# Performance work log

Measured on AMD Instinct MI355X. Metric: run time of the kernel, lower is better.

## Reference

```python
import jax, jax.numpy as jnp
import numpy as np

B, T, F, E, H = 1024, 128, 32, 16, 20
EPS = 1e-3  # keras BatchNormalization default epsilon
D = T * F   # flatten dim; fc1 builds with units = T*F due to pre-build units mutation


def lstm_relu(x, Wk, Wr, b, return_seq):
    """Keras LSTM with activation='relu', recurrent_activation=sigmoid.
    Gate order i, f, c(g), o. x: [B,T,Fin]. Returns [B,T,H] or [B,H]."""
    Bn = x.shape[0]
    h0 = jnp.zeros((Bn, H), x.dtype)
    c0 = jnp.zeros((Bn, H), x.dtype)

    def step(carry, xt):
        h, c = carry
        z = xt @ Wk + h @ Wr + b                      # [B, 4H]
        i, f, g, o = jnp.split(z, 4, axis=-1)
        i = jax.nn.sigmoid(i)
        f = jax.nn.sigmoid(f)
        g = jax.nn.relu(g)
        o = jax.nn.sigmoid(o)
        c = f * c + i * g
        h = o * jax.nn.relu(c)
        return (h, c), h

    (hT, _), hs = jax.lax.scan(step, (h0, c0), jnp.swapaxes(x, 0, 1))
    return jnp.swapaxes(hs, 0, 1) if return_seq else hT


def setup_inputs():
    key = jax.random.key(0)
    ks = jax.random.split(key, 16)
    s = 0.1
    d = {}
    d["x"] = jax.random.normal(ks[0], (B, T, F), jnp.float32)
    # BatchNorm (inference: moving stats)
    d["bn_gamma"] = jnp.ones((F,), jnp.float32)
    d["bn_beta"] = jnp.zeros((F,), jnp.float32)
    d["bn_mean"] = jax.random.normal(ks[1], (F,), jnp.float32) * 0.1
    d["bn_var"] = jax.random.uniform(ks[2], (F,), jnp.float32, 0.5, 1.5)
    # Per-expert LSTM stacks (stacked over expert axis E)
    d["k1"] = jax.random.normal(ks[3], (E, F, 4 * H), jnp.float32) * s
    d["r1"] = jax.random.normal(ks[4], (E, H, 4 * H), jnp.float32) * s
    d["b1"] = jnp.zeros((E, 4 * H), jnp.float32)
    d["k2"] = jax.random.normal(ks[5], (E, H, 4 * H), jnp.float32) * s
    d["r2"] = jax.random.normal(ks[6], (E, H, 4 * H), jnp.float32) * s
    d["b2"] = jnp.zeros((E, 4 * H), jnp.float32)
    d["dw"] = jax.random.normal(ks[7], (E, H, 1), jnp.float32) * s
    d["db"] = jnp.zeros((E, 1), jnp.float32)
    # Gating path: flatten -> Dense(D, relu) -> Dense(E, softmax)
    d["fc1_w"] = jax.random.normal(ks[8], (D, D), jnp.float32) * 0.02
    d["fc1_b"] = jnp.zeros((D,), jnp.float32)
    d["gate_w"] = jax.random.normal(ks[9], (D, E), jnp.float32) * 0.02
    d["gate_b"] = jnp.zeros((E,), jnp.float32)
    return d


def reference(x, bn_gamma, bn_beta, bn_mean, bn_var,
              k1, r1, b1, k2, r2, b2, dw, db,
              fc1_w, fc1_b, gate_w, gate_b):
    # BatchNorm (inference) over last axis
    xn = (x - bn_mean) * jax.lax.rsqrt(bn_var + EPS) * bn_gamma + bn_beta

    def run_expert(k1e, r1e, b1e, k2e, r2e, b2e, dwe, dbe):
        h1 = lstm_relu(xn, k1e, r1e, b1e, return_seq=True)    # [B,T,H]
        h2 = lstm_relu(h1, k2e, r2e, b2e, return_seq=False)   # [B,H]
        return h2 @ dwe + dbe                                  # [B,1]

    expert_outputs = jax.vmap(run_expert)(k1, r1, b1, k2, r2, b2, dw, db)  # [E,B,1]

    flat = x.reshape(x.shape[0], -1)                    # [B, T*F] (raw inputs, not normed)
    g = jax.nn.relu(flat @ fc1_w + fc1_b)               # [B, D]
    w = jax.nn.softmax(g @ gate_w + gate_b, axis=-1)    # [B, E]

    # stack(axis=1) -> [B,E,1]; weights expand_dims(axis=2) -> [B,E,1]; sum over E
    out = jnp.sum(jnp.transpose(expert_outputs, (1, 0, 2)) * w[:, :, None], axis=1)  # [B,1]
    return out
```

## Files before the change

kernel.cpp:

```cpp
#include <hip/hip_runtime.h>
#include <math.h>

#define Bsz 1024
#define Tt  128
#define Ff  32
#define Ee  16
#define Hh  20
#define Dd  4096
#define EPSc 1e-3f
#define LOG2E 1.4426950408889634f

#define PWE 7520

typedef __attribute__((ext_vector_type(8))) short bf16x8;
typedef __attribute__((ext_vector_type(4))) float f32x4;
typedef __attribute__((ext_vector_type(4))) unsigned int u32x4;

#define MFMA16(a,b,c) __builtin_amdgcn_mfma_f32_16x16x32_bf16(a, b, c, 0, 0, 0)

__device__ __forceinline__ float sig2(float z) {
    return __builtin_amdgcn_rcpf(1.0f + __builtin_amdgcn_exp2f(-z));
}
__device__ __forceinline__ unsigned short bf16_rne(float f) {
    unsigned u = __float_as_uint(f);
    u += 0x7FFFu + ((u >> 16) & 1u);
    return (unsigned short)(u >> 16);
}
__device__ __forceinline__ float bf16_to_f(unsigned short h) {
    return __uint_as_float(((unsigned)h) << 16);
}
__device__ __forceinline__ void cvt2(float f0, float f1, unsigned& hp, unsigned& lp) {
    asm("v_cvt_pk_bf16_f32 %0, %1, %2" : "=v"(hp) : "v"(f0), "v"(f1));
    float h0 = __uint_as_float(hp << 16);
    float h1 = __uint_as_float(hp & 0xFFFF0000u);
    asm("v_cvt_pk_bf16_f32 %0, %1, %2" : "=v"(lp) : "v"(f0 - h0), "v"(f1 - h1));
}

__global__ void xpack_kernel(const float* __restrict__ x,
                             const float* __restrict__ gamma, const float* __restrict__ beta,
                             const float* __restrict__ mean,  const float* __restrict__ var,
                             unsigned short* __restrict__ xph, unsigned short* __restrict__ xpl)
{
    __shared__ float sc[Ff], sh[Ff];
    int tid = threadIdx.x;
    if (tid < Ff) {
        float s = gamma[tid] * rsqrtf(var[tid] + EPSc);
        sc[tid] = s;
        sh[tid] = beta[tid] - mean[tid] * s;
    }
    __syncthreads();
    int idx = blockIdx.x * 256 + tid;
    int c   = idx >> 13;
    int rem = idx & 8191;
    int t   = rem >> 6;
    int l   = rem & 63;
    int q   = l >> 4, s = l & 15;
    const float* xr = x + ((size_t)(c * 16 + s) * Tt + t) * Ff + q * 8;
    float4 v0 = *(const float4*)xr;
    float4 v1 = *(const float4*)(xr + 4);
    float xv[8] = {v0.x, v0.y, v0.z, v0.w, v1.x, v1.y, v1.z, v1.w};
    bf16x8 hv, lv;
#pragma unroll
    for (int j = 0; j < 8; ++j) {
        int f = q * 8 + j;
        float xn_ = xv[j] * sc[f] + sh[f];
        unsigned short hi = bf16_rne(xn_);
        hv[j] = (short)hi;
        lv[j] = (short)bf16_rne(xn_ - bf16_to_f(hi));
    }
    *(bf16x8*)(xph + (size_t)idx * 8) = hv;
    *(bf16x8*)(xpl + (size_t)idx * 8) = lv;
}

__global__ void repack2_kernel(const float* __restrict__ k1, const float* __restrict__ r1,
                               const float* __restrict__ b1, const float* __restrict__ k2,
                               const float* __restrict__ r2, const float* __restrict__ b2,
                               float* __restrict__ pw)
{
    int idx = blockIdx.x * blockDim.x + threadIdx.x;
    if (idx >= Ee * PWE) return;
    int e = idx / PWE;
    int o = idx % PWE;
    float v;
    int g;
    if (o < 7360) {
        int c = o % 80, u = c >> 2;
        g = c & 3;
        int co = g * 20 + u;
        if (o < 2560) {
            int kk = o / 80;
            v = k1[((size_t)e * Ff + kk) * 80 + co];
        } else if (o < 4160) {
            int kk = (o - 2560) / 80;
            v = r1[((size_t)e * Hh + kk) * 80 + co];
        } else if (o < 5760) {
            int kk = (o - 4160) / 80;
            v = k2[((size_t)e * Hh + kk) * 80 + co];
        } else {
            int kk = (o - 5760) / 80;
            v = r2[((size_t)e * Hh + kk) * 80 + co];
        }
    } else if (o < 7440) {
        int c = o - 7360, u = c >> 2;
        g = c & 3;
        v = b1[(size_t)e * 80 + g * 20 + u];
    } else {
        int c = o - 7440, u = c >> 2;
        g = c & 3;
        v = b2[(size_t)e * 80 + g * 20 + u];
    }
    if (g != 2) v *= LOG2E;
    pw[idx] = v;
}

__global__ __launch_bounds__(256, 2) void fused_kernel(
    const unsigned short* __restrict__ xph, const unsigned short* __restrict__ xpl,
    const float* __restrict__ pw, const float* __restrict__ dw, const float* __restrict__ db,
    float* __restrict__ eo,
    const float* __restrict__ x, const float* __restrict__ W,
    const float* __restrict__ bias, float* __restrict__ C)
{
    __shared__ __align__(16) char smem[32768];

    if (blockIdx.x < 256) {
        const int l = threadIdx.x & 63;
        const int q = l >> 4, s = l & 15;
        const int tile = (blockIdx.x << 2) + (threadIdx.x >> 6);
        const int e = tile >> 6;
        const int c = tile & 63;
        const int b0 = c * 16;

        const float* Wm = pw + (size_t)e * PWE;
        bf16x8 K1h[5], K1l[5], R1h[5], R1l[5], K2h[5], K2l[5], R2h[5], R2l[5];
#pragma unroll
        for (int n = 0; n < 5; ++n) {
#pragma unroll
            for (int j = 0; j < 8; ++j) {
                int k8 = q * 8 + j;
                int uk = 4 * j + q;
                int cc = n * 16 + s;
                float wv_;
                unsigned short hi; float hf;
                wv_ = Wm[k8 * 80 + cc];
                hi = bf16_rne(wv_); hf = bf16_to_f(hi);
                K1h[n][j] = (short)hi; K1l[n][j] = (short)bf16_rne(wv_ - hf);
                wv_ = (j < 5) ? Wm[2560 + uk * 80 + cc] : 0.f;
                hi = bf16_rne(wv_); hf = bf16_to_f(hi);
                R1h[n][j] = (short)hi; R1l[n][j] = (short)bf16_rne(wv_ - hf);
                wv_ = (j < 5) ? Wm[4160 + uk * 80 + cc] : 0.f;
                hi = bf16_rne(wv_); hf = bf16_to_f(hi);
                K2h[n][j] = (short)hi; K2l[n][j] = (short)bf16_rne(wv_ - hf);
                wv_ = (j < 5) ? Wm[5760 + uk * 80 + cc] : 0.f;
                hi = bf16_rne(wv_); hf = bf16_to_f(hi);
                R2h[n][j] = (short)hi; R2l[n][j] = (short)bf16_rne(wv_ - hf);
            }
        }
        f32x4 bf1[5], bf2[5];
        float dwr[5];
#pragma unroll
        for (int n = 0; n < 5; ++n) {
            bf1[n] = *(const f32x4*)&Wm[7360 + n * 16 + 4 * q];
            bf2[n] = *(const f32x4*)&Wm[7440 + n * 16 + 4 * q];
            dwr[n] = dw[e * Hh + 4 * n + q];
        }

        float c1[5] = {0, 0, 0, 0, 0}, c2[5] = {0, 0, 0, 0, 0};
        float h2reg[5] = {0, 0, 0, 0, 0};

        const bf16x8 z8 = {0, 0, 0, 0, 0, 0, 0, 0};
        bf16x8 H1a = z8, H1b = z8, H2a = z8, H2b = z8;

        const unsigned short* xbh = xph + (size_t)c * 65536 + l * 8;
        const unsigned short* xbl = xpl + (size_t)c * 65536 + l * 8;
        bf16x8 xch = *(const bf16x8*)xbh;
        bf16x8 xcl = *(const bf16x8*)xbl;

#pragma unroll 1
        for (int t = 0; t < Tt; ++t) {
            bf16x8 xnh = xch, xnl = xcl;
            if (t < Tt - 1) {
                xnh = *(const bf16x8*)(xbh + (t + 1) * 512);
                xnl = *(const bf16x8*)(xbl + (t + 1) * 512);
            }

            f32x4 a1[5];
#pragma unroll
            for (int n = 0; n < 5; ++n) {
                f32x4 acc = bf1[n];
                acc = MFMA16(K1h[n], xch, acc);
                acc = MFMA16(K1l[n], xch, acc);
                acc = MFMA16(K1h[n], xcl, acc);
                acc = MFMA16(R1h[n], H1a, acc);
                acc = MFMA16(R1l[n], H1a, acc);
                acc = MFMA16(R1h[n], H1b, acc);
                a1[n] = acc;
            }
            {
                float hv[5];
#pragma unroll
                for (int n = 0; n < 5; ++n) {
                    float iv = sig2(a1[n][0]);
                    float fv = sig2(a1[n][1]);
                    float gv = fmaxf(a1[n][2], 0.f);
                    float ov = sig2(a1[n][3]);
                    c1[n] = fv * c1[n] + iv * gv;
                    hv[n] = ov * fmaxf(c1[n], 0.f);
                }
                unsigned h0, h1, h2, l0, l1, l2;
                cvt2(hv[0], hv[1], h0, l0);
                cvt2(hv[2], hv[3], h1, l1);
                cvt2(hv[4], 0.f,   h2, l2);
                u32x4 uh = {h0, h1, h2, 0u}, ul = {l0, l1, l2, 0u};
                H1a = __builtin_bit_cast(bf16x8, uh);
                H1b = __builtin_bit_cast(bf16x8, ul);
            }

            f32x4 a2[5];
#pragma unroll
            for (int n = 0; n < 5; ++n) {
                f32x4 acc = bf2[n];
                acc = MFMA16(R2h[n], H2a, acc);
                acc = MFMA16(R2l[n], H2a, acc);
                acc = MFMA16(R2h[n], H2b, acc);
                acc = MFMA16(K2h[n], H1a, acc);
                acc = MFMA16(K2l[n], H1a, acc);
                acc = MFMA16(K2h[n], H1b, acc);
                a2[n] = acc;
            }
            {
                float hv[5];
#pragma unroll
                for (int n = 0; n < 5; ++n) {
                    float iv = sig2(a2[n][0]);
                    float fv = sig2(a2[n][1]);
                    float gv = fmaxf(a2[n][2], 0.f);
                    float ov = sig2(a2[n][3]);
                    c2[n] = fv * c2[n] + iv * gv;
                    float h = ov * fmaxf(c2[n], 0.f);
                    h2reg[n] = h;
                    hv[n] = h;
                }
                unsigned h0, h1, h2, l0, l1, l2;
                cvt2(hv[0], hv[1], h0, l0);
                cvt2(hv[2], hv[3], h1, l1);
                cvt2(hv[4], 0.f,   h2, l2);
                u32x4 uh = {h0, h1, h2, 0u}, ul = {l0, l1, l2, 0u};
                H2a = __builtin_bit_cast(bf16x8, uh);
                H2b = __builtin_bit_cast(bf16x8, ul);
            }

            xch = xnh; xcl = xnl;
        }

        float p = 0.f;
#pragma unroll
        for (int n = 0; n < 5; ++n) p += h2reg[n] * dwr[n];
        p += __shfl_xor(p, 16);
        p += __shfl_xor(p, 32);
        if (q == 0) eo[(size_t)e * Bsz + b0 + s] = db[e] + p;

    } else {
        const int tid = threadIdx.x;
        const int wv = tid >> 6, l = tid & 63, q = l >> 4, s = l & 15;
        const int id = blockIdx.x & 255;
        const int n0 = (id & 31) * 128, m0 = (id >> 5) * 128;
        const int wr = (wv & 1) * 64, wc = (wv >> 1) * 64;

        const int wn = tid & 127, wkq = tid >> 7;
        const int r7w = wn & 7;
        const int pw0 = ((2 * wkq)     ^ r7w) * 8;
        const int pw1 = ((2 * wkq + 1) ^ r7w) * 8;
        const int pw2 = ((4 + 2 * wkq) ^ r7w) * 8;
        const int pw3 = ((5 + 2 * wkq) ^ r7w) * 8;

        const float* WG = W + (size_t)(wkq * 16) * Dd + n0 + wn;
        const float* Arow = x + (size_t)(m0 + wr + s) * Dd + q * 8;

        unsigned short* lds = (unsigned short*)smem;

        f32x4 acc[4][4];
#pragma unroll
        for (int mt = 0; mt < 4; ++mt)
#pragma unroll
            for (int nt = 0; nt < 4; ++nt) acc[mt][nt] = (f32x4){0.f, 0.f, 0.f, 0.f};

        float wfp[16];
        float4 afc[8];

        {
            float w0[16];
#pragma unroll
            for (int i = 0; i < 16; ++i) w0[i] = WG[(size_t)i * Dd];
            uint4 h0, l0, h1, l1;
            cvt2(w0[0],  w0[1],  h0.x, l0.x); cvt2(w0[2],  w0[3],  h0.y, l0.y);
            cvt2(w0[4],  w0[5],  h0.z, l0.z); cvt2(w0[6],  w0[7],  h0.w, l0.w);
            cvt2(w0[8],  w0[9],  h1.x, l1.x); cvt2(w0[10], w0[11], h1.y, l1.y);
            cvt2(w0[12], w0[13], h1.z, l1.z); cvt2(w0[14], w0[15], h1.w, l1.w);
            unsigned short* rb = lds + wn * 64;
            *(uint4*)&rb[pw0] = h0;
            *(uint4*)&rb[pw1] = h1;
            *(uint4*)&rb[pw2] = l0;
            *(uint4*)&rb[pw3] = l1;
#pragma unroll
            for (int i = 0; i < 16; ++i) wfp[i] = WG[(size_t)(32 + i) * Dd];
#pragma unroll
            for (int mt = 0; mt < 4; ++mt) {
                afc[mt * 2]     = *(const float4*)(Arow + (size_t)mt * 16 * Dd);
                afc[mt * 2 + 1] = *(const float4*)(Arow + (size_t)mt * 16 * Dd + 4);
            }
            __syncthreads();
        }

#pragma unroll 1
        for (int it = 0; it < 128; ++it) {
            const int k0 = it * 32;
            unsigned short* cb = lds + (it & 1) * 8192;
            unsigned short* sb = lds + ((it & 1) ^ 1) * 8192;

            if (it < 127) {
                uint4 h0, l0, h1, l1;
                cvt2(wfp[0],  wfp[1],  h0.x, l0.x); cvt2(wfp[2],  wfp[3],  h0.y, l0.y);
                cvt2(wfp[4],  wfp[5],  h0.z, l0.z); cvt2(wfp[6],  wfp[7],  h0.w, l0.w);
                cvt2(wfp[8],  wfp[9],  h1.x, l1.x); cvt2(wfp[10], wfp[11], h1.y, l1.y);
                cvt2(wfp[12], wfp[13], h1.z, l1.z); cvt2(wfp[14], wfp[15], h1.w, l1.w);
                unsigned short* rb = sb + wn * 64;
                *(uint4*)&rb[pw0] = h0;
                *(uint4*)&rb[pw1] = h1;
                *(uint4*)&rb[pw2] = l0;
                *(uint4*)&rb[pw3] = l1;
            }

            {
                const int kW = (it + 2 < 128) ? k0 + 64 : k0;
#pragma unroll
                for (int i = 0; i < 16; ++i) wfp[i] = WG[(size_t)(kW + i) * Dd];
            }

            bf16x8 Wfh[4], Wfl[4];
            {
                const int r7r = s & 7;
                const int ph = (q ^ r7r) * 8;
                const int pl = ((4 + q) ^ r7r) * 8;
#pragma unroll
                for (int nt = 0; nt < 4; ++nt) {
                    const unsigned short* rb = cb + (wc + nt * 16 + s) * 64;
                    Wfh[nt] = *(bf16x8*)&rb[ph];
                    Wfl[nt] = *(bf16x8*)&rb[pl];
                }
            }

            bf16x8 Afh[4], Afl[4];
#pragma unroll
            for (int mt = 0; mt < 4; ++mt) {
                uint4 uh, ul;
                cvt2(afc[mt * 2].x,     afc[mt * 2].y,     uh.x, ul.x);
                cvt2(afc[mt * 2].z,     afc[mt * 2].w,     uh.y, ul.y);
                cvt2(afc[mt * 2 + 1].x, afc[mt * 2 + 1].y, uh.z, ul.z);
                cvt2(afc[mt * 2 + 1].z, afc[mt * 2 + 1].w, uh.w, ul.w);
                Afh[mt] = __builtin_bit_cast(bf16x8, uh);
                Afl[mt] = __builtin_bit_cast(bf16x8, ul);
            }
            {
                const int kA = (it + 1 < 128) ? k0 + 32 : k0;
#pragma unroll
                for (int mt = 0; mt < 4; ++mt) {
                    afc[mt * 2]     = *(const float4*)(Arow + (size_t)mt * 16 * Dd + kA);
                    afc[mt * 2 + 1] = *(const float4*)(Arow + (size_t)mt * 16 * Dd + kA + 4);
                }
            }

#pragma unroll
            for (int mt = 0; mt < 4; ++mt)
#pragma unroll
                for (int nt = 0; nt < 4; ++nt) {
                    f32x4 a = acc[mt][nt];
                    a = MFMA16(Afl[mt], Wfh[nt], a);
                    a = MFMA16(Afh[mt], Wfl[nt], a);
                    a = MFMA16(Afh[mt], Wfh[nt], a);
                    acc[mt][nt] = a;
                }

            __syncthreads();
        }

#pragma unroll
        for (int nt = 0; nt < 4; ++nt) {
            float bv = bias[n0 + wc + nt * 16 + s];
#pragma unroll
            for (int mt = 0; mt < 4; ++mt)
#pragma unroll
                for (int r = 0; r < 4; ++r) {
                    int m = m0 + wr + mt * 16 + q * 4 + r;
                    C[(size_t)m * Dd + n0 + wc + nt * 16 + s] = fmaxf(acc[mt][nt][r] + bv, 0.f);
                }
        }
    }
}

__global__ __launch_bounds__(256) void gate_kernel(const float* __restrict__ g,
                                                   const float* __restrict__ gw,
                                                   const float* __restrict__ gb,
                                                   const float* __restrict__ eo,
                                                   float* __restrict__ out)
{
    int b0 = blockIdx.x * 4;
    int tid = threadIdx.x;
    int lane = tid & 63;
    int wv = tid >> 6;

    float acc[4][16];
#pragma unroll
    for (int bb = 0; bb < 4; ++bb)
#pragma unroll
        for (int j = 0; j < 16; ++j) acc[bb][j] = 0.f;

    const float* g0 = g + (size_t)b0 * Dd;
#pragma unroll
    for (int it = 0; it < Dd / 256; ++it) {
        int d = tid + it * 256;
        const float4* wr_ = (const float4*)(gw + (size_t)d * 16);
        float4 w0 = wr_[0], w1 = wr_[1], w2 = wr_[2], w3 = wr_[3];
        float gv[4];
#pragma unroll
        for (int bb = 0; bb < 4; ++bb) gv[bb] = g0[(size_t)bb * Dd + d];
#pragma unroll
        for (int bb = 0; bb < 4; ++bb) {
            float v = gv[bb];
            acc[bb][0]  += v * w0.x;  acc[bb][1]  += v * w0.y;
            acc[bb][2]  += v * w0.z;  acc[bb][3]  += v * w0.w;
            acc[bb][4]  += v * w1.x;  acc[bb][5]  += v * w1.y;
            acc[bb][6]  += v * w1.z;  acc[bb][7]  += v * w1.w;
            acc[bb][8]  += v * w2.x;  acc[bb][9]  += v * w2.y;
            acc[bb][10] += v * w2.z;  acc[bb][11] += v * w2.w;
            acc[bb][12] += v * w3.x;  acc[bb][13] += v * w3.y;
            acc[bb][14] += v * w3.z;  acc[bb][15] += v * w3.w;
        }
    }

    __shared__ float red[4][4][16];
    __shared__ float logits[4][16];
#pragma unroll
    for (int bb = 0; bb < 4; ++bb)
#pragma unroll
        for (int j = 0; j < 16; ++j) {
            float v = acc[bb][j];
#pragma unroll
            for (int m = 32; m >= 1; m >>= 1) v += __shfl_xor(v, m);
            if (lane == 0) red[wv][bb][j] = v;
        }
    __syncthreads();
    if (tid < 64) {
        int bb = tid >> 4, j = tid & 15;
        logits[bb][j] = gb[j] + red[0][bb][j] + red[1][bb][j] + red[2][bb][j] + red[3][bb][j];
    }
    __syncthreads();
    if (tid < 4) {
        int b = b0 + tid;
        float m = logits[tid][0];
#pragma unroll
        for (int j = 1; j < 16; ++j) m = fmaxf(m, logits[tid][j]);
        float ex[16], ssum = 0.f;
#pragma unroll
        for (int j = 0; j < 16; ++j) { ex[j] = __expf(logits[tid][j] - m); ssum += ex[j]; }
        float inv = 1.f / ssum;
        float o = 0.f;
#pragma unroll
        for (int j = 0; j < 16; ++j) o += ex[j] * inv * eo[(size_t)j * Bsz + b];
        out[b] = o;
    }
}

extern "C" void kernel_launch(void* const* d_in, const int* in_sizes, int n_in,
                              void* d_out, int out_size, void* d_ws, size_t ws_size,
                              hipStream_t stream)
{
    const float* x     = (const float*)d_in[0];
    const float* gamma = (const float*)d_in[1];
    const float* beta  = (const float*)d_in[2];
    const float* mean  = (const float*)d_in[3];
    const float* var   = (const float*)d_in[4];
    const float* k1    = (const float*)d_in[5];
    const float* r1    = (const float*)d_in[6];
    const float* b1    = (const float*)d_in[7];
    const float* k2    = (const float*)d_in[8];
    const float* r2    = (const float*)d_in[9];
    const float* b2    = (const float*)d_in[10];
    const float* dw    = (const float*)d_in[11];
    const float* db    = (const float*)d_in[12];
    const float* fc1w  = (const float*)d_in[13];
    const float* fc1b  = (const float*)d_in[14];
    const float* gw    = (const float*)d_in[15];
    const float* gb    = (const float*)d_in[16];
    float* out = (float*)d_out;

    float* g = (float*)d_ws;
    unsigned short* xph = (unsigned short*)(g + (size_t)Bsz * Dd);
    unsigned short* xpl = xph + (size_t)Bsz * Dd / 2 * 2;
    float* pw  = (float*)(xpl + (size_t)4194304);
    float* eo  = pw + (size_t)Ee * PWE;

    xpack_kernel<<<2048, 256, 0, stream>>>(x, gamma, beta, mean, var, xph, xpl);
    repack2_kernel<<<(Ee * PWE + 255) / 256, 256, 0, stream>>>(k1, r1, b1, k2, r2, b2, pw);
    fused_kernel<<<512, 256, 0, stream>>>(xph, xpl, pw, dw, db, eo, x, fc1w, fc1b, g);
    gate_kernel<<<Bsz / 4, 256, 0, stream>>>(g, gw, gb, eo, out);
}
```

Baseline: 450.0 us.

## Stage GEMM A tiles through LDS with deeper prefetch and merge prep kernels

The fc1 GEMM path now converts and stages the A operand (raw x) into LDS alongside W, rather than each wave converting its own A fragments from registers. Global loads run two k-steps ahead using two register sets, with the loop unrolled by two over double-buffered LDS. The LDS allocation doubles to 64KB and register pressure rises, which can reduce occupancy for the LSTM blocks that share this kernel. The xpack and weight repack kernels are also merged into a single launch to save one kernel launch.

```diff
diff --git a/kernel.cpp b/kernel.cpp
--- a/kernel.cpp
+++ b/kernel.cpp
@@ -36,81 +36,81 @@
     asm("v_cvt_pk_bf16_f32 %0, %1, %2" : "=v"(lp) : "v"(f0 - h0), "v"(f1 - h1));
 }
 
-__global__ void xpack_kernel(const float* __restrict__ x,
-                             const float* __restrict__ gamma, const float* __restrict__ beta,
-                             const float* __restrict__ mean,  const float* __restrict__ var,
-                             unsigned short* __restrict__ xph, unsigned short* __restrict__ xpl)
+__global__ void prep_kernel(const float* __restrict__ x,
+                            const float* __restrict__ gamma, const float* __restrict__ beta,
+                            const float* __restrict__ mean,  const float* __restrict__ var,
+                            unsigned short* __restrict__ xph, unsigned short* __restrict__ xpl,
+                            const float* __restrict__ k1, const float* __restrict__ r1,
+                            const float* __restrict__ b1, const float* __restrict__ k2,
+                            const float* __restrict__ r2, const float* __restrict__ b2,
+                            float* __restrict__ pw)
 {
-    __shared__ float sc[Ff], sh[Ff];
     int tid = threadIdx.x;
-    if (tid < Ff) {
-        float s = gamma[tid] * rsqrtf(var[tid] + EPSc);
-        sc[tid] = s;
-        sh[tid] = beta[tid] - mean[tid] * s;
+    if (blockIdx.x < 2048) {
+        __shared__ float sc[Ff], sh[Ff];
+        if (tid < Ff) {
+            float s = gamma[tid] * rsqrtf(var[tid] + EPSc);
+            sc[tid] = s;
+            sh[tid] = beta[tid] - mean[tid] * s;
+        }
+        __syncthreads();
+        int idx = blockIdx.x * 256 + tid;
+        int c   = idx >> 13;
+        int rem = idx & 8191;
+        int t   = rem >> 6;
+        int l   = rem & 63;
+        int q   = l >> 4, s = l & 15;
+        const float* xr = x + ((size_t)(c * 16 + s) * Tt + t) * Ff + q * 8;
+        float4 v0 = *(const float4*)xr;
+        float4 v1 = *(const float4*)(xr + 4);
+        float xv[8] = {v0.x, v0.y, v0.z, v0.w, v1.x, v1.y, v1.z, v1.w};
+        bf16x8 hv, lv;
+#pragma unroll
+        for (int j = 0; j < 8; ++j) {
+            int f = q * 8 + j;
+            float xn_ = xv[j] * sc[f] + sh[f];
+            unsigned short hi = bf16_rne(xn_);
+            hv[j] = (short)hi;
+            lv[j] = (short)bf16_rne(xn_ - bf16_to_f(hi));
+        }
+        *(bf16x8*)(xph + (size_t)idx * 8) = hv;
+        *(bf16x8*)(xpl + (size_t)idx * 8) = lv;
+    } else {
+        int idx = (blockIdx.x - 2048) * 256 + tid;
+        if (idx >= Ee * PWE) return;
+        int e = idx / PWE;
+        int o = idx % PWE;
+        float v;
+        int g;
+        if (o < 7360) {
+            int c = o % 80, u = c >> 2;
+            g = c & 3;
+            int co = g * 20 + u;
+            if (o < 2560) {
+                int kk = o / 80;
+                v = k1[((size_t)e * Ff + kk) * 80 + co];
+            } else if (o < 4160) {
+                int kk = (o - 2560) / 80;
+                v = r1[((size_t)e * Hh + kk) * 80 + co];
+            } else if (o < 5760) {
+                int kk = (o - 4160) / 80;
+                v = k2[((size_t)e * Hh + kk) * 80 + co];
+            } else {
+                int kk = (o - 5760) / 80;
+                v = r2[((size_t)e * Hh + kk) * 80 + co];
+            }
+        } else if (o < 7440) {
+            int c = o - 7360, u = c >> 2;
+            g = c & 3;
+            v = b1[(size_t)e * 80 + g * 20 + u];
+        } else {
+            int c = o - 7440, u = c >> 2;
+            g = c & 3;
+            v = b2[(size_t)e * 80 + g * 20 + u];
+        }
+        if (g != 2) v *= LOG2E;
+        pw[idx] = v;
     }
-    __syncthreads();
-    int idx = blockIdx.x * 256 + tid;
-    int c   = idx >> 13;
-    int rem = idx & 8191;
-    int t   = rem >> 6;
-    int l   = rem & 63;
-    int q   = l >> 4, s = l & 15;
-    const float* xr = x + ((size_t)(c * 16 + s) * Tt + t) * Ff + q * 8;
-    float4 v0 = *(const float4*)xr;
-    float4 v1 = *(const float4*)(xr + 4);
-    float xv[8] = {v0.x, v0.y, v0.z, v0.w, v1.x, v1.y, v1.z, v1.w};
-    bf16x8 hv, lv;
-#pragma unroll
-    for (int j = 0; j < 8; ++j) {
-        int f = q * 8 + j;
-        float xn_ = xv[j] * sc[f] + sh[f];
-        unsigned short hi = bf16_rne(xn_);
-        hv[j] = (short)hi;
-        lv[j] = (short)bf16_rne(xn_ - bf16_to_f(hi));
-    }
-    *(bf16x8*)(xph + (size_t)idx * 8) = hv;
-    *(bf16x8*)(xpl + (size_t)idx * 8) = lv;
-}
-
-__global__ void repack2_kernel(const float* __restrict__ k1, const float* __restrict__ r1,
-                               const float* __restrict__ b1, const float* __restrict__ k2,
-                               const float* __restrict__ r2, const float* __restrict__ b2,
-                               float* __restrict__ pw)
-{
-    int idx = blockIdx.x * blockDim.x + threadIdx.x;
-    if (idx >= Ee * PWE) return;
-    int e = idx / PWE;
-    int o = idx % PWE;
-    float v;
-    int g;
-    if (o < 7360) {
-        int c = o % 80, u = c >> 2;
-        g = c & 3;
-        int co = g * 20 + u;
-        if (o < 2560) {
-            int kk = o / 80;
-            v = k1[((size_t)e * Ff + kk) * 80 + co];
-        } else if (o < 4160) {
-            int kk = (o - 2560) / 80;
-            v = r1[((size_t)e * Hh + kk) * 80 + co];
-        } else if (o < 5760) {
-            int kk = (o - 4160) / 80;
-            v = k2[((size_t)e * Hh + kk) * 80 + co];
-        } else {
-            int kk = (o - 5760) / 80;
-            v = r2[((size_t)e * Hh + kk) * 80 + co];
-        }
-    } else if (o < 7440) {
-        int c = o - 7360, u = c >> 2;
-        g = c & 3;
-        v = b1[(size_t)e * 80 + g * 20 + u];
-    } else {
-        int c = o - 7440, u = c >> 2;
-        g = c & 3;
-        v = b2[(size_t)e * 80 + g * 20 + u];
-    }
-    if (g != 2) v *= LOG2E;
-    pw[idx] = v;
 }
 
 __global__ __launch_bounds__(256, 2) void fused_kernel(
@@ -120,7 +120,7 @@
     const float* __restrict__ x, const float* __restrict__ W,
     const float* __restrict__ bias, float* __restrict__ C)
 {
-    __shared__ __align__(16) char smem[32768];
+    __shared__ __align__(16) char smem[65536];
 
     if (blockIdx.x < 256) {
         const int l = threadIdx.x & 63;
@@ -272,11 +272,21 @@
         const int pw1 = ((2 * wkq + 1) ^ r7w) * 8;
         const int pw2 = ((4 + 2 * wkq) ^ r7w) * 8;
         const int pw3 = ((5 + 2 * wkq) ^ r7w) * 8;
-
         const float* WG = W + (size_t)(wkq * 16) * Dd + n0 + wn;
-        const float* Arow = x + (size_t)(m0 + wr + s) * Dd + q * 8;
+
+        const int ar = tid >> 3, ac = tid & 7;
+        const int akc = ac >> 1, ahalf = ac & 1;
+        const int pa_h = ((akc       ^ (ar & 7)) << 3) + ahalf * 4;
+        const int pa_l = (((4 + akc) ^ (ar & 7)) << 3) + ahalf * 4;
+        const float* AG = x + (size_t)(m0 + ar) * Dd + 4 * ac;
+
+        const int r7r = s & 7;
+        const int pfh = (q ^ r7r) * 8;
+        const int pfl = ((4 + q) ^ r7r) * 8;
 
         unsigned short* lds = (unsigned short*)smem;
+        unsigned short* c0 = lds;
+        unsigned short* c1 = lds + 16384;
 
         f32x4 acc[4][4];
 #pragma unroll
@@ -284,104 +294,108 @@
 #pragma unroll
             for (int nt = 0; nt < 4; ++nt) acc[mt][nt] = (f32x4){0.f, 0.f, 0.f, 0.f};
 
-        float wfp[16];
-        float4 afc[8];
+        float wA[16], wB[16];
+        float4 aA[4], aB[4];
+
+#define LOADW(dst, kk)                                                     \
+        {                                                                  \
+            const int kw_ = (kk);                                          \
+            _Pragma("unroll")                                              \
+            for (int i_ = 0; i_ < 16; ++i_)                                \
+                dst[i_] = WG[(size_t)(kw_ + i_) * Dd];                     \
+        }
+#define LOADA(dst, kk)                                                     \
+        {                                                                  \
+            const int ka_ = (kk);                                          \
+            _Pragma("unroll")                                              \
+            for (int p_ = 0; p_ < 4; ++p_)                                 \
+                dst[p_] = *(const float4*)(AG + (size_t)(32 * p_) * Dd + ka_); \
+        }
+#define STAGEW(dst, src)                                                   \
+        {                                                                  \
+            uint4 h0, l0, h1, l1;                                          \
+            cvt2(src[0],  src[1],  h0.x, l0.x); cvt2(src[2],  src[3],  h0.y, l0.y); \
+            cvt2(src[4],  src[5],  h0.z, l0.z); cvt2(src[6],  src[7],  h0.w, l0.w); \
+            cvt2(src[8],  src[9],  h1.x, l1.x); cvt2(src[10], src[11], h1.y, l1.y); \
+            cvt2(src[12], src[13], h1.z, l1.z); cvt2(src[14], src[15], h1.w, l1.w); \
+            unsigned short* rb_ = (dst) + wn * 64;                         \
+            *(uint4*)&rb_[pw0] = h0;                                       \
+            *(uint4*)&rb_[pw1] = h1;                                       \
+            *(uint4*)&rb_[pw2] = l0;                                       \
+            *(uint4*)&rb_[pw3] = l1;                                       \
+        }
+#define STAGEA(dst, src)                                                   \
+        {                                                                  \
+            _Pragma("unroll")                                              \
+            for (int p_ = 0; p_ < 4; ++p_) {                               \
+                unsigned h0_, l0_, h1_, l1_;                               \
+                cvt2(src[p_].x, src[p_].y, h0_, l0_);                      \
+                cvt2(src[p_].z, src[p_].w, h1_, l1_);                      \
+                unsigned short* rb_ = (dst) + 8192 + (ar + 32 * p_) * 64;  \
+                uint2 hv_ = {h0_, h1_}, lv_ = {l0_, l1_};                  \
+                *(uint2*)&rb_[pa_h] = hv_;                                 \
+                *(uint2*)&rb_[pa_l] = lv_;                                 \
+            }                                                              \
+        }
+#define COMPUTE(cb)                                                        \
+        {                                                                  \
+            bf16x8 Wfh[4], Wfl[4], Afh[4], Afl[4];                         \
+            _Pragma("unroll")                                              \
+            for (int nt = 0; nt < 4; ++nt) {                               \
+                const unsigned short* rb_ = (cb) + (wc + nt * 16 + s) * 64; \
+                Wfh[nt] = *(bf16x8*)&rb_[pfh];                             \
+                Wfl[nt] = *(bf16x8*)&rb_[pfl];                             \
+            }                                                              \
+            _Pragma("unroll")                                              \
+            for (int mt = 0; mt < 4; ++mt) {                               \
+                const unsigned short* ra_ = (cb) + 8192 + (wr + mt * 16 + s) * 64; \
+                Afh[mt] = *(bf16x8*)&ra_[pfh];                             \
+                Afl[mt] = *(bf16x8*)&ra_[pfl];                             \
+            }                                                              \
+            _Pragma("unroll")                                              \
+            for (int mt = 0; mt < 4; ++mt)                                 \
+                _Pragma("unroll")                                          \
+                for (int nt = 0; nt < 4; ++nt) {                           \
+                    f32x4 a_ = acc[mt][nt];                                \
+                    a_ = MFMA16(Afl[mt], Wfh[nt], a_);                     \
+                    a_ = MFMA16(Afh[mt], Wfl[nt], a_);                     \
+                    a_ = MFMA16(Afh[mt], Wfh[nt], a_);                     \
+                    acc[mt][nt] = a_;                                      \
+                }                                                          \
+        }
 
         {
-            float w0[16];
-#pragma unroll
-            for (int i = 0; i < 16; ++i) w0[i] = WG[(size_t)i * Dd];
-            uint4 h0, l0, h1, l1;
-            cvt2(w0[0],  w0[1],  h0.x, l0.x); cvt2(w0[2],  w0[3],  h0.y, l0.y);
-            cvt2(w0[4],  w0[5],  h0.z, l0.z); cvt2(w0[6],  w0[7],  h0.w, l0.w);
-            cvt2(w0[8],  w0[9],  h1.x, l1.x); cvt2(w0[10], w0[11], h1.y, l1.y);
-            cvt2(w0[12], w0[13], h1.z, l1.z); cvt2(w0[14], w0[15], h1.w, l1.w);
-            unsigned short* rb = lds + wn * 64;
-            *(uint4*)&rb[pw0] = h0;
-            *(uint4*)&rb[pw1] = h1;
-            *(uint4*)&rb[pw2] = l0;
-            *(uint4*)&rb[pw3] = l1;
-#pragma unroll
-            for (int i = 0; i < 16; ++i) wfp[i] = WG[(size_t)(32 + i) * Dd];
-#pragma unroll
-            for (int mt = 0; mt < 4; ++mt) {
-                afc[mt * 2]     = *(const float4*)(Arow + (size_t)mt * 16 * Dd);
-                afc[mt * 2 + 1] = *(const float4*)(Arow + (size_t)mt * 16 * Dd + 4);
-            }
+            float w0[16]; float4 a0[4];
+            LOADW(w0, 0); LOADA(a0, 0);
+            STAGEW(c0, w0); STAGEA(c0, a0);
+            LOADW(wA, 32); LOADA(aA, 32);
+            LOADW(wB, 64); LOADA(aB, 64);
             __syncthreads();
         }
 
 #pragma unroll 1
-        for (int it = 0; it < 128; ++it) {
-            const int k0 = it * 32;
-            unsigned short* cb = lds + (it & 1) * 8192;
-            unsigned short* sb = lds + ((it & 1) ^ 1) * 8192;
-
-            if (it < 127) {
-                uint4 h0, l0, h1, l1;
-                cvt2(wfp[0],  wfp[1],  h0.x, l0.x); cvt2(wfp[2],  wfp[3],  h0.y, l0.y);
-                cvt2(wfp[4],  wfp[5],  h0.z, l0.z); cvt2(wfp[6],  wfp[7],  h0.w, l0.w);
-                cvt2(wfp[8],  wfp[9],  h1.x, l1.x); cvt2(wfp[10], wfp[11], h1.y, l1.y);
-                cvt2(wfp[12], wfp[13], h1.z, l1.z); cvt2(wfp[14], wfp[15], h1.w, l1.w);
-                unsigned short* rb = sb + wn * 64;
-                *(uint4*)&rb[pw0] = h0;
-                *(uint4*)&rb[pw1] = h1;
-                *(uint4*)&rb[pw2] = l0;
-                *(uint4*)&rb[pw3] = l1;
-            }
-
+        for (int it = 0; it < 128; it += 2) {
+            STAGEW(c1, wA); STAGEA(c1, aA);
             {
-                const int kW = (it + 2 < 128) ? k0 + 64 : k0;
-#pragma unroll
-                for (int i = 0; i < 16; ++i) wfp[i] = WG[(size_t)(kW + i) * Dd];
-            }
-
-            bf16x8 Wfh[4], Wfl[4];
+                const int kk = (it + 3 < 128) ? (it + 3) * 32 : 0;
+                LOADW(wA, kk); LOADA(aA, kk);
+            }
+            COMPUTE(c0);
+            __syncthreads();
+
+            if (it + 2 < 128) { STAGEW(c0, wB); STAGEA(c0, aB); }
             {
-                const int r7r = s & 7;
-                const int ph = (q ^ r7r) * 8;
-                const int pl = ((4 + q) ^ r7r) * 8;
-#pragma unroll
-                for (int nt = 0; nt < 4; ++nt) {
-                    const unsigned short* rb = cb + (wc + nt * 16 + s) * 64;
-                    Wfh[nt] = *(bf16x8*)&rb[ph];
-                    Wfl[nt] = *(bf16x8*)&rb[pl];
-                }
-            }
-
-            bf16x8 Afh[4], Afl[4];
-#pragma unroll
-            for (int mt = 0; mt < 4; ++mt) {
-                uint4 uh, ul;
-                cvt2(afc[mt * 2].x,     afc[mt * 2].y,     uh.x, ul.x);
-                cvt2(afc[mt * 2].z,     afc[mt * 2].w,     uh.y, ul.y);
-                cvt2(afc[mt * 2 + 1].x, afc[mt * 2 + 1].y, uh.z, ul.z);
-                cvt2(afc[mt * 2 + 1].z, afc[mt * 2 + 1].w, uh.w, ul.w);
-                Afh[mt] = __builtin_bit_cast(bf16x8, uh);
-                Afl[mt] = __builtin_bit_cast(bf16x8, ul);
-            }
-            {
-                const int kA = (it + 1 < 128) ? k0 + 32 : k0;
-#pragma unroll
-                for (int mt = 0; mt < 4; ++mt) {
-                    afc[mt * 2]     = *(const float4*)(Arow + (size_t)mt * 16 * Dd + kA);
-                    afc[mt * 2 + 1] = *(const float4*)(Arow + (size_t)mt * 16 * Dd + kA + 4);
-                }
-            }
-
-#pragma unroll
-            for (int mt = 0; mt < 4; ++mt)
-#pragma unroll
-                for (int nt = 0; nt < 4; ++nt) {
-                    f32x4 a = acc[mt][nt];
-                    a = MFMA16(Afl[mt], Wfh[nt], a);
-                    a = MFMA16(Afh[mt], Wfl[nt], a);
-                    a = MFMA16(Afh[mt], Wfh[nt], a);
-                    acc[mt][nt] = a;
-                }
-
+                const int kk = (it + 4 < 128) ? (it + 4) * 32 : 0;
+                LOADW(wB, kk); LOADA(aB, kk);
+            }
+            COMPUTE(c1);
             __syncthreads();
         }
+#undef LOADW
+#undef LOADA
+#undef STAGEW
+#undef STAGEA
+#undef COMPUTE
 
 #pragma unroll
         for (int nt = 0; nt < 4; ++nt) {
@@ -499,8 +513,8 @@
     float* pw  = (float*)(xpl + (size_t)4194304);
     float* eo  = pw + (size_t)Ee * PWE;
 
-    xpack_kernel<<<2048, 256, 0, stream>>>(x, gamma, beta, mean, var, xph, xpl);
-    repack2_kernel<<<(Ee * PWE + 255) / 256, 256, 0, stream>>>(k1, r1, b1, k2, r2, b2, pw);
+    prep_kernel<<<2048 + (Ee * PWE + 255) / 256, 256, 0, stream>>>(
+        x, gamma, beta, mean, var, xph, xpl, k1, r1, b1, k2, r2, b2, pw);
     fused_kernel<<<512, 256, 0, stream>>>(xph, xpl, pw, dw, db, eo, x, fc1w, fc1b, g);
     gate_kernel<<<Bsz / 4, 256, 0, stream>>>(g, gw, gb, eo, out);
 }
```

New measurement: 401.5 us. 1.12x faster.
